# Kernel tuning notes

Measured on AMD Instinct MI355X. Metric: run time of the kernel, lower is better.

Reference implementation:

```python
import jax, jax.numpy as jnp
import numpy as np

C_IN, C_OUT, K = 64, 64, 3
KK = K * K


def _conv3x3(x, w, b):
    # x: [B, Cin, H, W], w: [Cout, Cin, 3, 3], b: [Cout] or None. stride 1, pad 1.
    y = jax.lax.conv_general_dilated(
        x, w, window_strides=(1, 1), padding=((1, 1), (1, 1)),
        dimension_numbers=("NCHW", "OIHW", "NCHW"))
    if b is not None:
        y = y + b[None, :, None, None]
    return y


def _deform_conv2d(x, offset, mask, weight):
    # torchvision.ops.deform_conv2d with stride=1, pad=1, dilation=1, 1 offset group.
    # x: [B,C,H,W]; offset: [B,2*KK,H,W] (per-tap (dy,dx)); mask: [B,KK,H,W];
    # weight: [O,C,K,K]
    B, C, H, W = x.shape
    O = weight.shape[0]
    ky, kx = jnp.meshgrid(jnp.arange(K), jnp.arange(K), indexing="ij")
    hs = jnp.arange(H)
    ws = jnp.arange(W)
    # base sample positions per tap k=(ky*K+kx): [KK,H,W]
    base_y = (hs[:, None] - 1)[None] + ky.reshape(KK, 1, 1)
    base_x = (ws[None, :] - 1)[None] + kx.reshape(KK, 1, 1)
    off = offset.reshape(B, KK, 2, H, W)
    py = base_y[None].astype(x.dtype) + off[:, :, 0]  # [B,KK,H,W]
    px = base_x[None].astype(x.dtype) + off[:, :, 1]

    y0 = jnp.floor(py)
    x0 = jnp.floor(px)
    wy = py - y0  # bilinear fractional weights
    wx = px - x0
    y0i = y0.astype(jnp.int32)
    x0i = x0.astype(jnp.int32)

    imflat = x.reshape(B, C, H * W)

    def gather_b(im, idx):  # im: [C,HW], idx: [KK,H,W] -> [C,KK,H,W]
        return im[:, idx]

    val = jnp.zeros((B, C, KK, H, W), x.dtype)
    for dy, dx in ((0, 0), (0, 1), (1, 0), (1, 1)):
        yc = y0i + dy
        xc = x0i + dx
        valid = ((yc >= 0) & (yc < H) & (xc >= 0) & (xc < W)).astype(x.dtype)
        cw = (wy if dy else (1.0 - wy)) * (wx if dx else (1.0 - wx)) * valid
        idx = jnp.clip(yc, 0, H - 1) * W + jnp.clip(xc, 0, W - 1)
        g = jax.vmap(gather_b)(imflat, idx)  # [B,C,KK,H,W]
        val = val + cw[:, None] * g
    val = val * mask[:, None]  # modulation
    # contract 9-tap patches with conv weight
    return jnp.einsum("bckhw,ock->bohw", val, weight.reshape(O, C, KK))


def setup_inputs() -> dict:
    key = jax.random.key(0)
    ks = jax.random.split(key, 8)
    B, H, W = 4, 96, 96
    cin2 = 2 * C_IN + 2
    frame_i = jax.random.normal(ks[0], (B, C_IN, H, W), jnp.float32)
    frame_j = jax.random.normal(ks[1], (B, C_IN, H, W), jnp.float32)
    flow_ij = jax.random.normal(ks[2], (B, 2, H, W), jnp.float32)
    # small random weights so offsets are nonzero (zero-init would degenerate)
    w_off = jax.random.normal(ks[3], (2 * KK, cin2, K, K), jnp.float32) * 0.01
    b_off = jax.random.normal(ks[4], (2 * KK,), jnp.float32) * 0.1
    w_mod = jax.random.normal(ks[5], (KK, cin2, K, K), jnp.float32) * 0.01
    b_mod = jax.random.normal(ks[6], (KK,), jnp.float32) * 0.1
    w_reg = jax.random.normal(ks[7], (C_OUT, C_IN, K, K), jnp.float32) * (1.0 / np.sqrt(C_IN * KK))
    return {"frame_i": frame_i, "frame_j": frame_j, "flow_ij": flow_ij,
            "w_off": w_off, "b_off": b_off, "w_mod": w_mod, "b_mod": b_mod,
            "w_reg": w_reg}


def reference(frame_i, frame_j, flow_ij, w_off, b_off, w_mod, b_mod, w_reg):
    offset_input = jnp.concatenate([frame_i, frame_j, flow_ij], axis=1)
    offset = _conv3x3(offset_input, w_off, b_off)            # [B,2*KK,H,W]
    modulator = 2.0 * jax.nn.sigmoid(_conv3x3(offset_input, w_mod, b_mod))  # [B,KK,H,W]
    return _deform_conv2d(frame_j, offset, modulator, w_reg)
```

## Files before the change

kernel.cpp:

```cpp
#include <hip/hip_runtime.h>
#include <math.h>

#define BB   4
#define HH   96
#define WW   96
#define HW   (HH * WW)
#define CIN  64
#define COUT 64
#define NPL  17
#define HWP  (HW + 1)
#define NROW (BB * HW)
#define NSTRIP (NROW / 16)
#define BPX3 (NSTRIP / 8)
#define NA   (9 * 5 * 2 * 512)
#define NW   (9 * 2 * 4 * 512)
#define PXB2 (NROW / 32)
#define PWBLK 324
#define TSX  35
#define NIT  (NPL * 54)

typedef short v8s __attribute__((ext_vector_type(8)));
typedef float v4f __attribute__((ext_vector_type(4)));

__device__ __forceinline__ unsigned short f2bf(float f) {
    unsigned u = __float_as_uint(f);
    return (unsigned short)((u + 0x7FFFu + ((u >> 16) & 1u)) >> 16);
}
__device__ __forceinline__ unsigned pack2(float a, float b) {
    return (unsigned)f2bf(a) | ((unsigned)f2bf(b) << 16);
}
__device__ __forceinline__ unsigned bil2(unsigned a, unsigned b, unsigned c,
                                         unsigned d, float w00, float w01,
                                         float w10, float w11) {
    float lo = w00 * __uint_as_float(a << 16) + w01 * __uint_as_float(b << 16)
             + w10 * __uint_as_float(c << 16) + w11 * __uint_as_float(d << 16);
    float hi = w00 * __uint_as_float(a & 0xffff0000u)
             + w01 * __uint_as_float(b & 0xffff0000u)
             + w10 * __uint_as_float(c & 0xffff0000u)
             + w11 * __uint_as_float(d & 0xffff0000u);
    return pack2(lo, hi);
}

__global__ __launch_bounds__(256) void prep_kernel(
    const float* __restrict__ fi, const float* __restrict__ fj,
    const float* __restrict__ fl, const float* __restrict__ w_off,
    const float* __restrict__ w_mod, const float* __restrict__ w_reg,
    uint4* __restrict__ xp, unsigned short* __restrict__ wa2f,
    unsigned short* __restrict__ wb2f)
{
    int blk = blockIdx.x;
    if (blk < PXB2) {
        __shared__ __align__(16) unsigned tile[64 * TSX];
        int tid = threadIdx.x;
        int p = tid & 63, cg = tid >> 6;
        int u = blk >> 1, half = blk & 1;
        int r0 = u * 64;
        int b = r0 / HW;
        int hwb = r0 - b * HW;
        int hw = hwb + p;
        uint4* xpb = xp + (size_t)b * NPL * HWP;
        if (half == 0) {
            const float* pi = fi + (size_t)b * CIN * HW + hw;
#pragma unroll
            for (int d = 0; d < 8; ++d) {
                int c = cg * 16 + 2 * d;
                tile[p * TSX + cg * 8 + d] =
                    pack2(pi[(size_t)c * HW], pi[(size_t)(c + 1) * HW]);
            }
            __syncthreads();
#pragma unroll
            for (int i = 0; i < 2; ++i) {
                int it = i * 256 + tid;
                int pl = it >> 6, rl = it & 63;
                const unsigned* s = &tile[rl * TSX + pl * 4];
                uint4 v = {s[0], s[1], s[2], s[3]};
                xpb[(size_t)pl * HWP + hwb + rl] = v;
            }
        } else {
            const float* pj = fj + (size_t)b * CIN * HW + hw;
#pragma unroll
            for (int d = 0; d < 8; ++d) {
                int c = cg * 16 + 2 * d;
                tile[p * TSX + cg * 8 + d] =
                    pack2(pj[(size_t)c * HW], pj[(size_t)(c + 1) * HW]);
            }
            if (cg == 0) {
                const float* pf = fl + (size_t)b * 2 * HW + hw;
                tile[p * TSX + 32] = pack2(pf[0], pf[HW]);
            }
            __syncthreads();
#pragma unroll
            for (int i = 0; i < 2; ++i) {
                int it = i * 256 + tid;
                int pl = it >> 6, rl = it & 63;
                int o  = (pl >> 1) + (pl & 1) * 4;
                const unsigned* s = &tile[rl * TSX + o * 4];
                uint4 v = {s[0], s[1], s[2], s[3]};
                xpb[(size_t)(8 + pl) * HWP + hwb + rl] = v;
            }
            if (tid < 64) {
                uint4 v = {tile[tid * TSX + 32], 0u, 0u, 0u};
                xpb[(size_t)16 * HWP + hwb + tid] = v;
            }
        }
    } else if (blk < PXB2 + PWBLK) {
        int e = (blk - PXB2) * 256 + threadIdx.x;
        if (e < NA) {
            int t  = e / 5120;
            int r1 = e - t * 5120;
            int ks = r1 >> 10;
            int r2 = r1 & 1023;
            int nt = r2 >> 9;
            int l9 = r2 & 511;
            int l  = l9 >> 3, ee = l9 & 7;
            int m  = l & 15, g = l >> 4;
            int oc = nt * 16 + m;
            int ch = ks * 32 + g * 8 + ee;
            float v = 0.0f;
            if (oc < 27 && ch < 130) {
                if (oc < 18) v = w_off[((size_t)oc * 130 + ch) * 9 + t];
                else         v = w_mod[((size_t)(oc - 18) * 130 + ch) * 9 + t];
            }
            wa2f[e] = f2bf(v);
        } else {
            int e2 = e - NA;
            if (e2 < NW) {
                int k  = e2 >> 12;
                int r1 = e2 & 4095;
                int ks = r1 >> 11;
                int r2 = r1 & 2047;
                int nt = r2 >> 9;
                int l9 = r2 & 511;
                int l  = l9 >> 3, ee = l9 & 7;
                int m  = l & 15, g = l >> 4;
                int o  = nt * 16 + m;
                int c  = ks * 32 + g * 8 + ee;
                wb2f[e2] = f2bf(w_reg[((size_t)o * 64 + c) * 9 + k]);
            }
        }
    } else {
        if (threadIdx.x < BB * NPL) {
            int bz = threadIdx.x / NPL, pl = threadIdx.x - bz * NPL;
            uint4 z = {0u, 0u, 0u, 0u};
            xp[((size_t)bz * NPL + pl) * HWP + HW] = z;
        }
    }
}

__global__ __launch_bounds__(512, 8) void fused_kernel(
    const uint4* __restrict__ xp,
    const unsigned short* __restrict__ wa2f,
    const unsigned short* __restrict__ wb2f,
    const float* __restrict__ b_off, const float* __restrict__ b_mod,
    float* __restrict__ out)
{
    __shared__ __align__(16) unsigned char pool[16384];
    __shared__ __align__(16) float red1[8][8][64];
    __shared__ float lraw[16 * 28];

    uint4* patchL = (uint4*)pool;
    float* red2   = (float*)pool;

    int tid = threadIdx.x;
    int l = tid & 63;
    int wid = __builtin_amdgcn_readfirstlane(tid >> 6);
    int m = l & 15, g = l >> 4;
    int strip = (blockIdx.x & 7) * BPX3 + (blockIdx.x >> 3);
    int b = strip / (HW / 16);
    int hw0 = (strip - b * (HW / 16)) * 16;
    int hw = hw0 + m;
    int x = hw % WW, y = hw / WW;
    int y0b = hw0 / WW, x0b = hw0 - y0b * WW;

    const uint4* xpb = xp + (size_t)b * NPL * HWP;

#pragma unroll
    for (int i = 0; i < 2; ++i) {
        int item = i * 512 + tid;
        if (item < NIT) {
            int pl  = item / 54;
            int rm  = item - pl * 54;
            int run = rm / 18;
            int r18 = rm - run * 18;
            int yy = y0b + run - 1;
            int xx = x0b - 1 + r18;
            bool ok = ((unsigned)yy < HH) && ((unsigned)xx < WW);
            int pos = ok ? (yy * WW + xx) : HW;
            patchL[item] = xpb[(size_t)pl * HWP + pos];
        }
    }
    __syncthreads();

    v4f acc0 = {0.f, 0.f, 0.f, 0.f};
    v4f acc1 = {0.f, 0.f, 0.f, 0.f};
    {
        int nu = (wid < 5) ? 6 : 5;
#pragma unroll
        for (int i = 0; i < 6; ++i) {
            if (i < nu) {
                int u = wid + 8 * i;
                int t = u / 5, ks = u - 5 * t;
                int r = (t / 3) * 18 + (t % 3) + m;
                v8s a;
                if (ks == 4) {
                    uint4 t4 = patchL[16 * 54 + r];
                    if (g) t4 = (uint4){0u, 0u, 0u, 0u};
                    a = __builtin_bit_cast(v8s, t4);
                } else {
                    int pl = (ks == 0) ? g : (ks == 1) ? 4 + g
                           : (ks == 2) ? 8 + 2 * g : 9 + 2 * g;
                    a = *(const v8s*)&patchL[pl * 54 + r];
                }
                const unsigned short* wp =
                    wa2f + ((size_t)(u * 2)) * 512 + l * 8;
                v8s b0 = *(const v8s*)(wp);
                v8s b1 = *(const v8s*)(wp + 512);
                acc0 = __builtin_amdgcn_mfma_f32_16x16x32_bf16(a, b0, acc0, 0, 0, 0);
                acc1 = __builtin_amdgcn_mfma_f32_16x16x32_bf16(a, b1, acc1, 0, 0, 0);
            }
        }
    }

    {
#pragma unroll
        for (int j = 0; j < 4; ++j) red1[wid][j][l] = acc0[j];
#pragma unroll
        for (int j = 0; j < 4; ++j) red1[wid][4 + j][l] = acc1[j];
    }
    __syncthreads();

    {
        int j = wid;
        float v = 0.f;
#pragma unroll
        for (int sw = 0; sw < 8; ++sw) v += red1[sw][j][l];
        int r = j & 3;
        int oc = (j < 4) ? m : 16 + m;
        int pos = g * 4 + r;
        if (oc < 18) {
            lraw[pos * 28 + oc] = v + b_off[oc];
        } else if (oc < 27) {
            lraw[pos * 28 + oc] =
                2.0f / (1.0f + __expf(-(v + b_mod[oc - 18])));
        }
    }
    __syncthreads();

    v4f acc[4];
#pragma unroll
    for (int nt = 0; nt < 4; ++nt) acc[nt] = (v4f){0.f, 0.f, 0.f, 0.f};

    auto do_tap = [&](int k) {
        int ky = k / 3, kx = k - 3 * ky;
        float dy = lraw[m * 28 + 2 * k];
        float dx = lraw[m * 28 + 2 * k + 1];
        float mm = lraw[m * 28 + 18 + k];

        float py = (float)(y - 1 + ky) + dy;
        float px = (float)(x - 1 + kx) + dx;
        float fy = floorf(py), fx = floorf(px);
        int   y0 = (int)fy,    x0 = (int)fx;
        float wy = py - fy,    wx = px - fx;
        int   y1 = y0 + 1,     x1 = x0 + 1;

        bool y0v = (y0 >= 0) && (y0 < HH);
        bool y1v = (y1 >= 0) && (y1 < HH);
        bool x0v = (x0 >= 0) && (x0 < WW);
        bool x1v = (x1 >= 0) && (x1 < WW);

        float w00 = (1.f - wy) * (1.f - wx) * ((y0v && x0v) ? mm : 0.f);
        float w01 = (1.f - wy) * wx         * ((y0v && x1v) ? mm : 0.f);
        float w10 = wy * (1.f - wx)         * ((y1v && x0v) ? mm : 0.f);
        float w11 = wy * wx                 * ((y1v && x1v) ? mm : 0.f);

        int y0c = min(max(y0, 0), HH - 1), y1c = min(max(y1, 0), HH - 1);
        int x0c = min(max(x0, 0), WW - 1), x1c = min(max(x1, 0), WW - 1);
        int i00 = y0c * WW + x0c, i01 = y0c * WW + x1c;
        int i10 = y1c * WW + x0c, i11 = y1c * WW + x1c;

        const uint4* p0 = xpb + (size_t)(8 + 2 * g) * HWP;
        const uint4* p1 = p0 + HWP;

        uint4 a00 = p0[i00];
        uint4 a01 = p0[i01];
        uint4 a10 = p0[i10];
        uint4 a11 = p0[i11];
        uint4 c00 = p1[i00];
        uint4 c01 = p1[i01];
        uint4 c10 = p1[i10];
        uint4 c11 = p1[i11];

        uint4 ov0, ov1;
        ov0.x = bil2(a00.x, a01.x, a10.x, a11.x, w00, w01, w10, w11);
        ov0.y = bil2(a00.y, a01.y, a10.y, a11.y, w00, w01, w10, w11);
        ov0.z = bil2(a00.z, a01.z, a10.z, a11.z, w00, w01, w10, w11);
        ov0.w = bil2(a00.w, a01.w, a10.w, a11.w, w00, w01, w10, w11);
        ov1.x = bil2(c00.x, c01.x, c10.x, c11.x, w00, w01, w10, w11);
        ov1.y = bil2(c00.y, c01.y, c10.y, c11.y, w00, w01, w10, w11);
        ov1.z = bil2(c00.z, c01.z, c10.z, c11.z, w00, w01, w10, w11);
        ov1.w = bil2(c00.w, c01.w, c10.w, c11.w, w00, w01, w10, w11);
        v8s af0 = __builtin_bit_cast(v8s, ov0);
        v8s af1 = __builtin_bit_cast(v8s, ov1);

#pragma unroll
        for (int nt = 0; nt < 4; ++nt) {
            const unsigned short* wp0 =
                wb2f + ((size_t)((k * 2 + 0) * 4 + nt)) * 512 + l * 8;
            const unsigned short* wp1 =
                wb2f + ((size_t)((k * 2 + 1) * 4 + nt)) * 512 + l * 8;
            v8s bb0 = *(const v8s*)wp0;
            v8s bb1 = *(const v8s*)wp1;
            acc[nt] = __builtin_amdgcn_mfma_f32_16x16x32_bf16(af0, bb0, acc[nt], 0, 0, 0);
            acc[nt] = __builtin_amdgcn_mfma_f32_16x16x32_bf16(af1, bb1, acc[nt], 0, 0, 0);
        }
    };

    auto do_half = [&](int k, int ks) {
        int ky = k / 3, kx = k - 3 * ky;
        float dy = lraw[m * 28 + 2 * k];
        float dx = lraw[m * 28 + 2 * k + 1];
        float mm = lraw[m * 28 + 18 + k];

        float py = (float)(y - 1 + ky) + dy;
        float px = (float)(x - 1 + kx) + dx;
        float fy = floorf(py), fx = floorf(px);
        int   y0 = (int)fy,    x0 = (int)fx;
        float wy = py - fy,    wx = px - fx;
        int   y1 = y0 + 1,     x1 = x0 + 1;

        bool y0v = (y0 >= 0) && (y0 < HH);
        bool y1v = (y1 >= 0) && (y1 < HH);
        bool x0v = (x0 >= 0) && (x0 < WW);
        bool x1v = (x1 >= 0) && (x1 < WW);

        float w00 = (1.f - wy) * (1.f - wx) * ((y0v && x0v) ? mm : 0.f);
        float w01 = (1.f - wy) * wx         * ((y0v && x1v) ? mm : 0.f);
        float w10 = wy * (1.f - wx)         * ((y1v && x0v) ? mm : 0.f);
        float w11 = wy * wx                 * ((y1v && x1v) ? mm : 0.f);

        int y0c = min(max(y0, 0), HH - 1), y1c = min(max(y1, 0), HH - 1);
        int x0c = min(max(x0, 0), WW - 1), x1c = min(max(x1, 0), WW - 1);
        int i00 = y0c * WW + x0c, i01 = y0c * WW + x1c;
        int i10 = y1c * WW + x0c, i11 = y1c * WW + x1c;

        const uint4* pk = xpb + (size_t)(8 + 2 * g + ks) * HWP;
        uint4 a00 = pk[i00];
        uint4 a01 = pk[i01];
        uint4 a10 = pk[i10];
        uint4 a11 = pk[i11];

        uint4 ov;
        ov.x = bil2(a00.x, a01.x, a10.x, a11.x, w00, w01, w10, w11);
        ov.y = bil2(a00.y, a01.y, a10.y, a11.y, w00, w01, w10, w11);
        ov.z = bil2(a00.z, a01.z, a10.z, a11.z, w00, w01, w10, w11);
        ov.w = bil2(a00.w, a01.w, a10.w, a11.w, w00, w01, w10, w11);
        v8s af = __builtin_bit_cast(v8s, ov);

#pragma unroll
        for (int nt = 0; nt < 4; ++nt) {
            const unsigned short* wp =
                wb2f + ((size_t)((k * 2 + ks) * 4 + nt)) * 512 + l * 8;
            v8s bb = *(const v8s*)wp;
            acc[nt] = __builtin_amdgcn_mfma_f32_16x16x32_bf16(af, bb, acc[nt], 0, 0, 0);
        }
    };

    do_tap(wid);
    if (wid == 6) do_half(8, 0);
    if (wid == 7) do_half(8, 1);

    if (wid >= 4) {
        float* rb = red2 + ((size_t)(wid - 4) * 16) * 64;
#pragma unroll
        for (int nt = 0; nt < 4; ++nt)
#pragma unroll
            for (int r = 0; r < 4; ++r)
                rb[(nt * 4 + r) * 64 + l] = acc[nt][r];
    }
    __syncthreads();
    if (wid < 4) {
        float* rb = red2 + ((size_t)wid * 16) * 64;
#pragma unroll
        for (int nt = 0; nt < 4; ++nt)
#pragma unroll
            for (int r = 0; r < 4; ++r) {
                float t = rb[(nt * 4 + r) * 64 + l] + acc[nt][r];
                rb[(nt * 4 + r) * 64 + l] = t;
            }
    }
    __syncthreads();
    {
        int nt = wid >> 1, r0 = (wid & 1) * 2;
        float v0 = 0.f, v1 = 0.f;
#pragma unroll
        for (int bu = 0; bu < 4; ++bu) {
            v0 += red2[((size_t)bu * 16 + nt * 4 + r0) * 64 + l];
            v1 += red2[((size_t)bu * 16 + nt * 4 + r0 + 1) * 64 + l];
        }
        float* op = out + ((size_t)(b * COUT + nt * 16 + m)) * HW
                  + hw0 + g * 4 + r0;
        float2 s2 = {v0, v1};
        *(float2*)op = s2;
    }
}

extern "C" void kernel_launch(void* const* d_in, const int* in_sizes, int n_in,
                              void* d_out, int out_size, void* d_ws, size_t ws_size,
                              hipStream_t stream)
{
    const float* frame_i = (const float*)d_in[0];
    const float* frame_j = (const float*)d_in[1];
    const float* flow_ij = (const float*)d_in[2];
    const float* w_off   = (const float*)d_in[3];
    const float* b_off   = (const float*)d_in[4];
    const float* w_mod   = (const float*)d_in[5];
    const float* b_mod   = (const float*)d_in[6];
    const float* w_reg   = (const float*)d_in[7];
    float* out = (float*)d_out;

    uint4* xp = (uint4*)d_ws;
    unsigned short* wa2f = (unsigned short*)(xp + (size_t)BB * NPL * HWP);
    unsigned short* wb2f = wa2f + NA;

    prep_kernel<<<PXB2 + PWBLK + 1, 256, 0, stream>>>(
        frame_i, frame_j, flow_ij, w_off, w_mod, w_reg, xp, wa2f, wb2f);

    fused_kernel<<<NSTRIP, 512, 0, stream>>>(
        xp, wa2f, wb2f, b_off, b_mod, out);
}
```

Before: 112.1 us.

## Merge prep and fused kernels into persistent kernel with grid-wide barrier

Combines the bf16 repacking/weight-prep kernel and the deformable conv kernel into one persistent kernel of 384 blocks. The blocks first do the prep jobs in two halves, then meet at an atomic-counter grid barrier, then loop over the strips. This removes a kernel launch and the gap between launches. In exchange it adds a hipMemsetAsync, a spin barrier that relies on all blocks being resident at once, and lower occupancy from the launch bounds of 512 threads with 4 waves.

```diff
diff --git a/kernel.cpp b/kernel.cpp
--- a/kernel.cpp
+++ b/kernel.cpp
@@ -12,12 +12,14 @@
 #define NROW (BB * HW)
 #define NSTRIP (NROW / 16)
 #define BPX3 (NSTRIP / 8)
+#define GRIDN 384
 #define NA   (9 * 5 * 2 * 512)
 #define NW   (9 * 2 * 4 * 512)
 #define PXB2 (NROW / 32)
 #define PWBLK 324
 #define TSX  35
 #define NIT  (NPL * 54)
+#define CNT_OFF ((size_t)BB * NPL * HWP * 16 + (size_t)NA * 2 + (size_t)NW * 2)
 
 typedef short v8s __attribute__((ext_vector_type(8)));
 typedef float v4f __attribute__((ext_vector_type(4)));
@@ -41,366 +43,383 @@
     return pack2(lo, hi);
 }
 
-__global__ __launch_bounds__(256) void prep_kernel(
+__global__ __launch_bounds__(512, 4) void mono_kernel(
     const float* __restrict__ fi, const float* __restrict__ fj,
     const float* __restrict__ fl, const float* __restrict__ w_off,
     const float* __restrict__ w_mod, const float* __restrict__ w_reg,
+    const float* __restrict__ b_off, const float* __restrict__ b_mod,
     uint4* __restrict__ xp, unsigned short* __restrict__ wa2f,
-    unsigned short* __restrict__ wb2f)
+    unsigned short* __restrict__ wb2f, unsigned* __restrict__ cnt,
+    float* __restrict__ out)
 {
-    int blk = blockIdx.x;
-    if (blk < PXB2) {
-        __shared__ __align__(16) unsigned tile[64 * TSX];
-        int tid = threadIdx.x;
-        int p = tid & 63, cg = tid >> 6;
-        int u = blk >> 1, half = blk & 1;
+    __shared__ __align__(16) unsigned char pool[16384];
+    __shared__ __align__(16) float red1[8][8][64];
+    __shared__ float lraw[16 * 28];
+
+    int tid  = threadIdx.x;
+    int half = tid >> 8;
+    int stid = tid & 255;
+
+#pragma unroll 1
+    for (int it = 0; it < 2; ++it) {
+        int job = it * (GRIDN * 2) + (int)blockIdx.x * 2 + half;
+        unsigned* tile = half ? (unsigned*)red1 : (unsigned*)pool;
+        int p = stid & 63, cgp = stid >> 6;
+        bool isX = job < PXB2;
+        int u = job >> 1;
         int r0 = u * 64;
         int b = r0 / HW;
         int hwb = r0 - b * HW;
         int hw = hwb + p;
         uint4* xpb = xp + (size_t)b * NPL * HWP;
-        if (half == 0) {
+
+        if (isX && half == 0) {
             const float* pi = fi + (size_t)b * CIN * HW + hw;
 #pragma unroll
             for (int d = 0; d < 8; ++d) {
-                int c = cg * 16 + 2 * d;
-                tile[p * TSX + cg * 8 + d] =
+                int c = cgp * 16 + 2 * d;
+                tile[p * TSX + cgp * 8 + d] =
                     pack2(pi[(size_t)c * HW], pi[(size_t)(c + 1) * HW]);
             }
-            __syncthreads();
+        } else if (isX) {
+            const float* pj = fj + (size_t)b * CIN * HW + hw;
+#pragma unroll
+            for (int d = 0; d < 8; ++d) {
+                int c = cgp * 16 + 2 * d;
+                tile[p * TSX + cgp * 8 + d] =
+                    pack2(pj[(size_t)c * HW], pj[(size_t)(c + 1) * HW]);
+            }
+            if (cgp == 0) {
+                const float* pf = fl + (size_t)b * 2 * HW + hw;
+                tile[p * TSX + 32] = pack2(pf[0], pf[HW]);
+            }
+        } else if (job < PXB2 + PWBLK) {
+            int e = (job - PXB2) * 256 + stid;
+            if (e < NA) {
+                int t  = e / 5120;
+                int r1 = e - t * 5120;
+                int ks = r1 >> 10;
+                int r2 = r1 & 1023;
+                int nt = r2 >> 9;
+                int l9 = r2 & 511;
+                int l  = l9 >> 3, ee = l9 & 7;
+                int m  = l & 15, g = l >> 4;
+                int oc = nt * 16 + m;
+                int ch = ks * 32 + g * 8 + ee;
+                float v = 0.0f;
+                if (oc < 27 && ch < 130) {
+                    if (oc < 18) v = w_off[((size_t)oc * 130 + ch) * 9 + t];
+                    else         v = w_mod[((size_t)(oc - 18) * 130 + ch) * 9 + t];
+                }
+                wa2f[e] = f2bf(v);
+            } else {
+                int e2 = e - NA;
+                if (e2 < NW) {
+                    int k  = e2 >> 12;
+                    int r1 = e2 & 4095;
+                    int ks = r1 >> 11;
+                    int r2 = r1 & 2047;
+                    int nt = r2 >> 9;
+                    int l9 = r2 & 511;
+                    int l  = l9 >> 3, ee = l9 & 7;
+                    int m  = l & 15, g = l >> 4;
+                    int o  = nt * 16 + m;
+                    int c  = ks * 32 + g * 8 + ee;
+                    wb2f[e2] = f2bf(w_reg[((size_t)o * 64 + c) * 9 + k]);
+                }
+            }
+        } else if (job == PXB2 + PWBLK) {
+            if (stid < BB * NPL) {
+                int bz = stid / NPL, pl = stid - bz * NPL;
+                uint4 z = {0u, 0u, 0u, 0u};
+                xp[((size_t)bz * NPL + pl) * HWP + HW] = z;
+            }
+        }
+        __syncthreads();
+        if (isX && half == 0) {
 #pragma unroll
             for (int i = 0; i < 2; ++i) {
-                int it = i * 256 + tid;
-                int pl = it >> 6, rl = it & 63;
+                int it2 = i * 256 + stid;
+                int pl = it2 >> 6, rl = it2 & 63;
                 const unsigned* s = &tile[rl * TSX + pl * 4];
                 uint4 v = {s[0], s[1], s[2], s[3]};
                 xpb[(size_t)pl * HWP + hwb + rl] = v;
             }
-        } else {
-            const float* pj = fj + (size_t)b * CIN * HW + hw;
-#pragma unroll
-            for (int d = 0; d < 8; ++d) {
-                int c = cg * 16 + 2 * d;
-                tile[p * TSX + cg * 8 + d] =
-                    pack2(pj[(size_t)c * HW], pj[(size_t)(c + 1) * HW]);
-            }
-            if (cg == 0) {
-                const float* pf = fl + (size_t)b * 2 * HW + hw;
-                tile[p * TSX + 32] = pack2(pf[0], pf[HW]);
-            }
-            __syncthreads();
+        } else if (isX) {
 #pragma unroll
             for (int i = 0; i < 2; ++i) {
-                int it = i * 256 + tid;
-                int pl = it >> 6, rl = it & 63;
+                int it2 = i * 256 + stid;
+                int pl = it2 >> 6, rl = it2 & 63;
                 int o  = (pl >> 1) + (pl & 1) * 4;
                 const unsigned* s = &tile[rl * TSX + o * 4];
                 uint4 v = {s[0], s[1], s[2], s[3]};
                 xpb[(size_t)(8 + pl) * HWP + hwb + rl] = v;
             }
-            if (tid < 64) {
-                uint4 v = {tile[tid * TSX + 32], 0u, 0u, 0u};
-                xpb[(size_t)16 * HWP + hwb + tid] = v;
-            }
-        }
-    } else if (blk < PXB2 + PWBLK) {
-        int e = (blk - PXB2) * 256 + threadIdx.x;
-        if (e < NA) {
-            int t  = e / 5120;
-            int r1 = e - t * 5120;
-            int ks = r1 >> 10;
-            int r2 = r1 & 1023;
-            int nt = r2 >> 9;
-            int l9 = r2 & 511;
-            int l  = l9 >> 3, ee = l9 & 7;
-            int m  = l & 15, g = l >> 4;
-            int oc = nt * 16 + m;
-            int ch = ks * 32 + g * 8 + ee;
-            float v = 0.0f;
-            if (oc < 27 && ch < 130) {
-                if (oc < 18) v = w_off[((size_t)oc * 130 + ch) * 9 + t];
-                else         v = w_mod[((size_t)(oc - 18) * 130 + ch) * 9 + t];
-            }
-            wa2f[e] = f2bf(v);
-        } else {
-            int e2 = e - NA;
-            if (e2 < NW) {
-                int k  = e2 >> 12;
-                int r1 = e2 & 4095;
-                int ks = r1 >> 11;
-                int r2 = r1 & 2047;
-                int nt = r2 >> 9;
-                int l9 = r2 & 511;
-                int l  = l9 >> 3, ee = l9 & 7;
-                int m  = l & 15, g = l >> 4;
-                int o  = nt * 16 + m;
-                int c  = ks * 32 + g * 8 + ee;
-                wb2f[e2] = f2bf(w_reg[((size_t)o * 64 + c) * 9 + k]);
-            }
-        }
-    } else {
-        if (threadIdx.x < BB * NPL) {
-            int bz = threadIdx.x / NPL, pl = threadIdx.x - bz * NPL;
-            uint4 z = {0u, 0u, 0u, 0u};
-            xp[((size_t)bz * NPL + pl) * HWP + HW] = z;
-        }
+            if (stid < 64) {
+                uint4 v = {tile[stid * TSX + 32], 0u, 0u, 0u};
+                xpb[(size_t)16 * HWP + hwb + stid] = v;
+            }
+        }
+        __syncthreads();
     }
-}
-
-__global__ __launch_bounds__(512, 8) void fused_kernel(
-    const uint4* __restrict__ xp,
-    const unsigned short* __restrict__ wa2f,
-    const unsigned short* __restrict__ wb2f,
-    const float* __restrict__ b_off, const float* __restrict__ b_mod,
-    float* __restrict__ out)
-{
-    __shared__ __align__(16) unsigned char pool[16384];
-    __shared__ __align__(16) float red1[8][8][64];
-    __shared__ float lraw[16 * 28];
+
+    if (tid == 0) {
+        __threadfence();
+        __hip_atomic_fetch_add(cnt, 1u, __ATOMIC_ACQ_REL,
+                               __HIP_MEMORY_SCOPE_AGENT);
+        while (__hip_atomic_load(cnt, __ATOMIC_ACQUIRE,
+                                 __HIP_MEMORY_SCOPE_AGENT) < (unsigned)GRIDN)
+            __builtin_amdgcn_s_sleep(2);
+    }
+    __syncthreads();
 
     uint4* patchL = (uint4*)pool;
     float* red2   = (float*)pool;
 
-    int tid = threadIdx.x;
     int l = tid & 63;
     int wid = __builtin_amdgcn_readfirstlane(tid >> 6);
     int m = l & 15, g = l >> 4;
-    int strip = (blockIdx.x & 7) * BPX3 + (blockIdx.x >> 3);
-    int b = strip / (HW / 16);
-    int hw0 = (strip - b * (HW / 16)) * 16;
-    int hw = hw0 + m;
-    int x = hw % WW, y = hw / WW;
-    int y0b = hw0 / WW, x0b = hw0 - y0b * WW;
-
-    const uint4* xpb = xp + (size_t)b * NPL * HWP;
-
-#pragma unroll
-    for (int i = 0; i < 2; ++i) {
-        int item = i * 512 + tid;
-        if (item < NIT) {
-            int pl  = item / 54;
-            int rm  = item - pl * 54;
-            int run = rm / 18;
-            int r18 = rm - run * 18;
-            int yy = y0b + run - 1;
-            int xx = x0b - 1 + r18;
-            bool ok = ((unsigned)yy < HH) && ((unsigned)xx < WW);
-            int pos = ok ? (yy * WW + xx) : HW;
-            patchL[item] = xpb[(size_t)pl * HWP + pos];
-        }
-    }
-    __syncthreads();
-
-    v4f acc0 = {0.f, 0.f, 0.f, 0.f};
-    v4f acc1 = {0.f, 0.f, 0.f, 0.f};
-    {
-        int nu = (wid < 5) ? 6 : 5;
-#pragma unroll
-        for (int i = 0; i < 6; ++i) {
-            if (i < nu) {
-                int u = wid + 8 * i;
-                int t = u / 5, ks = u - 5 * t;
-                int r = (t / 3) * 18 + (t % 3) + m;
-                v8s a;
-                if (ks == 4) {
-                    uint4 t4 = patchL[16 * 54 + r];
-                    if (g) t4 = (uint4){0u, 0u, 0u, 0u};
-                    a = __builtin_bit_cast(v8s, t4);
-                } else {
-                    int pl = (ks == 0) ? g : (ks == 1) ? 4 + g
-                           : (ks == 2) ? 8 + 2 * g : 9 + 2 * g;
-                    a = *(const v8s*)&patchL[pl * 54 + r];
+
+#pragma unroll 1
+    for (int sj = (int)blockIdx.x; sj < NSTRIP; sj += GRIDN) {
+        int strip = (sj & 7) * BPX3 + (sj >> 3);
+        int b = strip / (HW / 16);
+        int hw0 = (strip - b * (HW / 16)) * 16;
+        int hw = hw0 + m;
+        int x = hw % WW, y = hw / WW;
+        int y0b = hw0 / WW, x0b = hw0 - y0b * WW;
+
+        const uint4* xpb = xp + (size_t)b * NPL * HWP;
+
+#pragma unroll
+        for (int i = 0; i < 2; ++i) {
+            int item = i * 512 + tid;
+            if (item < NIT) {
+                int pl  = item / 54;
+                int rm  = item - pl * 54;
+                int run = rm / 18;
+                int r18 = rm - run * 18;
+                int yy = y0b + run - 1;
+                int xx = x0b - 1 + r18;
+                bool ok = ((unsigned)yy < HH) && ((unsigned)xx < WW);
+                int pos = ok ? (yy * WW + xx) : HW;
+                patchL[item] = xpb[(size_t)pl * HWP + pos];
+            }
+        }
+        __syncthreads();
+
+        v4f acc0 = {0.f, 0.f, 0.f, 0.f};
+        v4f acc1 = {0.f, 0.f, 0.f, 0.f};
+        {
+            int nu = (wid < 5) ? 6 : 5;
+#pragma unroll
+            for (int i = 0; i < 6; ++i) {
+                if (i < nu) {
+                    int u = wid + 8 * i;
+                    int t = u / 5, ks = u - 5 * t;
+                    int r = (t / 3) * 18 + (t % 3) + m;
+                    v8s a;
+                    if (ks == 4) {
+                        uint4 t4 = patchL[16 * 54 + r];
+                        if (g) t4 = (uint4){0u, 0u, 0u, 0u};
+                        a = __builtin_bit_cast(v8s, t4);
+                    } else {
+                        int pl = (ks == 0) ? g : (ks == 1) ? 4 + g
+                               : (ks == 2) ? 8 + 2 * g : 9 + 2 * g;
+                        a = *(const v8s*)&patchL[pl * 54 + r];
+                    }
+                    const unsigned short* wp =
+                        wa2f + ((size_t)(u * 2)) * 512 + l * 8;
+                    v8s b0 = *(const v8s*)(wp);
+                    v8s b1 = *(const v8s*)(wp + 512);
+                    acc0 = __builtin_amdgcn_mfma_f32_16x16x32_bf16(a, b0, acc0, 0, 0, 0);
+                    acc1 = __builtin_amdgcn_mfma_f32_16x16x32_bf16(a, b1, acc1, 0, 0, 0);
                 }
+            }
+        }
+
+        {
+#pragma unroll
+            for (int j = 0; j < 4; ++j) red1[wid][j][l] = acc0[j];
+#pragma unroll
+            for (int j = 0; j < 4; ++j) red1[wid][4 + j][l] = acc1[j];
+        }
+        __syncthreads();
+
+        {
+            int j = wid;
+            float v = 0.f;
+#pragma unroll
+            for (int sw = 0; sw < 8; ++sw) v += red1[sw][j][l];
+            int r = j & 3;
+            int oc = (j < 4) ? m : 16 + m;
+            int pos = g * 4 + r;
+            if (oc < 18) {
+                lraw[pos * 28 + oc] = v + b_off[oc];
+            } else if (oc < 27) {
+                lraw[pos * 28 + oc] =
+                    2.0f / (1.0f + __expf(-(v + b_mod[oc - 18])));
+            }
+        }
+        __syncthreads();
+
+        v4f acc[4];
+#pragma unroll
+        for (int nt = 0; nt < 4; ++nt) acc[nt] = (v4f){0.f, 0.f, 0.f, 0.f};
+
+        auto do_tap = [&](int k) {
+            int ky = k / 3, kx = k - 3 * ky;
+            float dy = lraw[m * 28 + 2 * k];
+            float dx = lraw[m * 28 + 2 * k + 1];
+            float mm = lraw[m * 28 + 18 + k];
+
+            float py = (float)(y - 1 + ky) + dy;
+            float px = (float)(x - 1 + kx) + dx;
+            float fy = floorf(py), fx = floorf(px);
+            int   y0 = (int)fy,    x0 = (int)fx;
+            float wy = py - fy,    wx = px - fx;
+            int   y1 = y0 + 1,     x1 = x0 + 1;
+
+            bool y0v = (y0 >= 0) && (y0 < HH);
+            bool y1v = (y1 >= 0) && (y1 < HH);
+            bool x0v = (x0 >= 0) && (x0 < WW);
+            bool x1v = (x1 >= 0) && (x1 < WW);
+
+            float w00 = (1.f - wy) * (1.f - wx) * ((y0v && x0v) ? mm : 0.f);
+            float w01 = (1.f - wy) * wx         * ((y0v && x1v) ? mm : 0.f);
+            float w10 = wy * (1.f - wx)         * ((y1v && x0v) ? mm : 0.f);
+            float w11 = wy * wx                 * ((y1v && x1v) ? mm : 0.f);
+
+            int y0c = min(max(y0, 0), HH - 1), y1c = min(max(y1, 0), HH - 1);
+            int x0c = min(max(x0, 0), WW - 1), x1c = min(max(x1, 0), WW - 1);
+            int i00 = y0c * WW + x0c, i01 = y0c * WW + x1c;
+            int i10 = y1c * WW + x0c, i11 = y1c * WW + x1c;
+
+            const uint4* p0 = xpb + (size_t)(8 + 2 * g) * HWP;
+            const uint4* p1 = p0 + HWP;
+
+            uint4 a00 = p0[i00];
+            uint4 a01 = p0[i01];
+            uint4 a10 = p0[i10];
+            uint4 a11 = p0[i11];
+            uint4 c00 = p1[i00];
+            uint4 c01 = p1[i01];
+            uint4 c10 = p1[i10];
+            uint4 c11 = p1[i11];
+
+            uint4 ov0, ov1;
+            ov0.x = bil2(a00.x, a01.x, a10.x, a11.x, w00, w01, w10, w11);
+            ov0.y = bil2(a00.y, a01.y, a10.y, a11.y, w00, w01, w10, w11);
+            ov0.z = bil2(a00.z, a01.z, a10.z, a11.z, w00, w01, w10, w11);
+            ov0.w = bil2(a00.w, a01.w, a10.w, a11.w, w00, w01, w10, w11);
+            ov1.x = bil2(c00.x, c01.x, c10.x, c11.x, w00, w01, w10, w11);
+            ov1.y = bil2(c00.y, c01.y, c10.y, c11.y, w00, w01, w10, w11);
+            ov1.z = bil2(c00.z, c01.z, c10.z, c11.z, w00, w01, w10, w11);
+            ov1.w = bil2(c00.w, c01.w, c10.w, c11.w, w00, w01, w10, w11);
+            v8s af0 = __builtin_bit_cast(v8s, ov0);
+            v8s af1 = __builtin_bit_cast(v8s, ov1);
+
+#pragma unroll
+            for (int nt = 0; nt < 4; ++nt) {
+                const unsigned short* wp0 =
+                    wb2f + ((size_t)((k * 2 + 0) * 4 + nt)) * 512 + l * 8;
+                const unsigned short* wp1 =
+                    wb2f + ((size_t)((k * 2 + 1) * 4 + nt)) * 512 + l * 8;
+                v8s bb0 = *(const v8s*)wp0;
+                v8s bb1 = *(const v8s*)wp1;
+                acc[nt] = __builtin_amdgcn_mfma_f32_16x16x32_bf16(af0, bb0, acc[nt], 0, 0, 0);
+                acc[nt] = __builtin_amdgcn_mfma_f32_16x16x32_bf16(af1, bb1, acc[nt], 0, 0, 0);
+            }
+        };
+
+        auto do_half = [&](int k, int ks) {
+            int ky = k / 3, kx = k - 3 * ky;
+            float dy = lraw[m * 28 + 2 * k];
+            float dx = lraw[m * 28 + 2 * k + 1];
+            float mm = lraw[m * 28 + 18 + k];
+
+            float py = (float)(y - 1 + ky) + dy;
+            float px = (float)(x - 1 + kx) + dx;
+            float fy = floorf(py), fx = floorf(px);
+            int   y0 = (int)fy,    x0 = (int)fx;
+            float wy = py - fy,    wx = px - fx;
+            int   y1 = y0 + 1,     x1 = x0 + 1;
+
+            bool y0v = (y0 >= 0) && (y0 < HH);
+            bool y1v = (y1 >= 0) && (y1 < HH);
+            bool x0v = (x0 >= 0) && (x0 < WW);
+            bool x1v = (x1 >= 0) && (x1 < WW);
+
+            float w00 = (1.f - wy) * (1.f - wx) * ((y0v && x0v) ? mm : 0.f);
+            float w01 = (1.f - wy) * wx         * ((y0v && x1v) ? mm : 0.f);
+            float w10 = wy * (1.f - wx)         * ((y1v && x0v) ? mm : 0.f);
+            float w11 = wy * wx                 * ((y1v && x1v) ? mm : 0.f);
+
+            int y0c = min(max(y0, 0), HH - 1), y1c = min(max(y1, 0), HH - 1);
+            int x0c = min(max(x0, 0), WW - 1), x1c = min(max(x1, 0), WW - 1);
+            int i00 = y0c * WW + x0c, i01 = y0c * WW + x1c;
+            int i10 = y1c * WW + x0c, i11 = y1c * WW + x1c;
+
+            const uint4* pk = xpb + (size_t)(8 + 2 * g + ks) * HWP;
+            uint4 a00 = pk[i00];
+            uint4 a01 = pk[i01];
+            uint4 a10 = pk[i10];
+            uint4 a11 = pk[i11];
+
+            uint4 ov;
+            ov.x = bil2(a00.x, a01.x, a10.x, a11.x, w00, w01, w10, w11);
+            ov.y = bil2(a00.y, a01.y, a10.y, a11.y, w00, w01, w10, w11);
+            ov.z = bil2(a00.z, a01.z, a10.z, a11.z, w00, w01, w10, w11);
+            ov.w = bil2(a00.w, a01.w, a10.w, a11.w, w00, w01, w10, w11);
+            v8s af = __builtin_bit_cast(v8s, ov);
+
+#pragma unroll
+            for (int nt = 0; nt < 4; ++nt) {
                 const unsigned short* wp =
-                    wa2f + ((size_t)(u * 2)) * 512 + l * 8;
-                v8s b0 = *(const v8s*)(wp);
-                v8s b1 = *(const v8s*)(wp + 512);
-                acc0 = __builtin_amdgcn_mfma_f32_16x16x32_bf16(a, b0, acc0, 0, 0, 0);
-                acc1 = __builtin_amdgcn_mfma_f32_16x16x32_bf16(a, b1, acc1, 0, 0, 0);
-            }
-        }
-    }
-
-    {
-#pragma unroll
-        for (int j = 0; j < 4; ++j) red1[wid][j][l] = acc0[j];
-#pragma unroll
-        for (int j = 0; j < 4; ++j) red1[wid][4 + j][l] = acc1[j];
-    }
-    __syncthreads();
-
-    {
-        int j = wid;
-        float v = 0.f;
-#pragma unroll
-        for (int sw = 0; sw < 8; ++sw) v += red1[sw][j][l];
-        int r = j & 3;
-        int oc = (j < 4) ? m : 16 + m;
-        int pos = g * 4 + r;
-        if (oc < 18) {
-            lraw[pos * 28 + oc] = v + b_off[oc];
-        } else if (oc < 27) {
-            lraw[pos * 28 + oc] =
-                2.0f / (1.0f + __expf(-(v + b_mod[oc - 18])));
-        }
-    }
-    __syncthreads();
-
-    v4f acc[4];
-#pragma unroll
-    for (int nt = 0; nt < 4; ++nt) acc[nt] = (v4f){0.f, 0.f, 0.f, 0.f};
-
-    auto do_tap = [&](int k) {
-        int ky = k / 3, kx = k - 3 * ky;
-        float dy = lraw[m * 28 + 2 * k];
-        float dx = lraw[m * 28 + 2 * k + 1];
-        float mm = lraw[m * 28 + 18 + k];
-
-        float py = (float)(y - 1 + ky) + dy;
-        float px = (float)(x - 1 + kx) + dx;
-        float fy = floorf(py), fx = floorf(px);
-        int   y0 = (int)fy,    x0 = (int)fx;
-        float wy = py - fy,    wx = px - fx;
-        int   y1 = y0 + 1,     x1 = x0 + 1;
-
-        bool y0v = (y0 >= 0) && (y0 < HH);
-        bool y1v = (y1 >= 0) && (y1 < HH);
-        bool x0v = (x0 >= 0) && (x0 < WW);
-        bool x1v = (x1 >= 0) && (x1 < WW);
-
-        float w00 = (1.f - wy) * (1.f - wx) * ((y0v && x0v) ? mm : 0.f);
-        float w01 = (1.f - wy) * wx         * ((y0v && x1v) ? mm : 0.f);
-        float w10 = wy * (1.f - wx)         * ((y1v && x0v) ? mm : 0.f);
-        float w11 = wy * wx                 * ((y1v && x1v) ? mm : 0.f);
-
-        int y0c = min(max(y0, 0), HH - 1), y1c = min(max(y1, 0), HH - 1);
-        int x0c = min(max(x0, 0), WW - 1), x1c = min(max(x1, 0), WW - 1);
-        int i00 = y0c * WW + x0c, i01 = y0c * WW + x1c;
-        int i10 = y1c * WW + x0c, i11 = y1c * WW + x1c;
-
-        const uint4* p0 = xpb + (size_t)(8 + 2 * g) * HWP;
-        const uint4* p1 = p0 + HWP;
-
-        uint4 a00 = p0[i00];
-        uint4 a01 = p0[i01];
-        uint4 a10 = p0[i10];
-        uint4 a11 = p0[i11];
-        uint4 c00 = p1[i00];
-        uint4 c01 = p1[i01];
-        uint4 c10 = p1[i10];
-        uint4 c11 = p1[i11];
-
-        uint4 ov0, ov1;
-        ov0.x = bil2(a00.x, a01.x, a10.x, a11.x, w00, w01, w10, w11);
-        ov0.y = bil2(a00.y, a01.y, a10.y, a11.y, w00, w01, w10, w11);
-        ov0.z = bil2(a00.z, a01.z, a10.z, a11.z, w00, w01, w10, w11);
-        ov0.w = bil2(a00.w, a01.w, a10.w, a11.w, w00, w01, w10, w11);
-        ov1.x = bil2(c00.x, c01.x, c10.x, c11.x, w00, w01, w10, w11);
-        ov1.y = bil2(c00.y, c01.y, c10.y, c11.y, w00, w01, w10, w11);
-        ov1.z = bil2(c00.z, c01.z, c10.z, c11.z, w00, w01, w10, w11);
-        ov1.w = bil2(c00.w, c01.w, c10.w, c11.w, w00, w01, w10, w11);
-        v8s af0 = __builtin_bit_cast(v8s, ov0);
-        v8s af1 = __builtin_bit_cast(v8s, ov1);
-
-#pragma unroll
-        for (int nt = 0; nt < 4; ++nt) {
-            const unsigned short* wp0 =
-                wb2f + ((size_t)((k * 2 + 0) * 4 + nt)) * 512 + l * 8;
-            const unsigned short* wp1 =
-                wb2f + ((size_t)((k * 2 + 1) * 4 + nt)) * 512 + l * 8;
-            v8s bb0 = *(const v8s*)wp0;
-            v8s bb1 = *(const v8s*)wp1;
-            acc[nt] = __builtin_amdgcn_mfma_f32_16x16x32_bf16(af0, bb0, acc[nt], 0, 0, 0);
-            acc[nt] = __builtin_amdgcn_mfma_f32_16x16x32_bf16(af1, bb1, acc[nt], 0, 0, 0);
-        }
-    };
-
-    auto do_half = [&](int k, int ks) {
-        int ky = k / 3, kx = k - 3 * ky;
-        float dy = lraw[m * 28 + 2 * k];
-        float dx = lraw[m * 28 + 2 * k + 1];
-        float mm = lraw[m * 28 + 18 + k];
-
-        float py = (float)(y - 1 + ky) + dy;
-        float px = (float)(x - 1 + kx) + dx;
-        float fy = floorf(py), fx = floorf(px);
-        int   y0 = (int)fy,    x0 = (int)fx;
-        float wy = py - fy,    wx = px - fx;
-        int   y1 = y0 + 1,     x1 = x0 + 1;
-
-        bool y0v = (y0 >= 0) && (y0 < HH);
-        bool y1v = (y1 >= 0) && (y1 < HH);
-        bool x0v = (x0 >= 0) && (x0 < WW);
-        bool x1v = (x1 >= 0) && (x1 < WW);
-
-        float w00 = (1.f - wy) * (1.f - wx) * ((y0v && x0v) ? mm : 0.f);
-        float w01 = (1.f - wy) * wx         * ((y0v && x1v) ? mm : 0.f);
-        float w10 = wy * (1.f - wx)         * ((y1v && x0v) ? mm : 0.f);
-        float w11 = wy * wx                 * ((y1v && x1v) ? mm : 0.f);
-
-        int y0c = min(max(y0, 0), HH - 1), y1c = min(max(y1, 0), HH - 1);
-        int x0c = min(max(x0, 0), WW - 1), x1c = min(max(x1, 0), WW - 1);
-        int i00 = y0c * WW + x0c, i01 = y0c * WW + x1c;
-        int i10 = y1c * WW + x0c, i11 = y1c * WW + x1c;
-
-        const uint4* pk = xpb + (size_t)(8 + 2 * g + ks) * HWP;
-        uint4 a00 = pk[i00];
-        uint4 a01 = pk[i01];
-        uint4 a10 = pk[i10];
-        uint4 a11 = pk[i11];
-
-        uint4 ov;
-        ov.x = bil2(a00.x, a01.x, a10.x, a11.x, w00, w01, w10, w11);
-        ov.y = bil2(a00.y, a01.y, a10.y, a11.y, w00, w01, w10, w11);
-        ov.z = bil2(a00.z, a01.z, a10.z, a11.z, w00, w01, w10, w11);
-        ov.w = bil2(a00.w, a01.w, a10.w, a11.w, w00, w01, w10, w11);
-        v8s af = __builtin_bit_cast(v8s, ov);
-
-#pragma unroll
-        for (int nt = 0; nt < 4; ++nt) {
-            const unsigned short* wp =
-                wb2f + ((size_t)((k * 2 + ks) * 4 + nt)) * 512 + l * 8;
-            v8s bb = *(const v8s*)wp;
-            acc[nt] = __builtin_amdgcn_mfma_f32_16x16x32_bf16(af, bb, acc[nt], 0, 0, 0);
-        }
-    };
-
-    do_tap(wid);
-    if (wid == 6) do_half(8, 0);
-    if (wid == 7) do_half(8, 1);
-
-    if (wid >= 4) {
-        float* rb = red2 + ((size_t)(wid - 4) * 16) * 64;
-#pragma unroll
-        for (int nt = 0; nt < 4; ++nt)
-#pragma unroll
-            for (int r = 0; r < 4; ++r)
-                rb[(nt * 4 + r) * 64 + l] = acc[nt][r];
-    }
-    __syncthreads();
-    if (wid < 4) {
-        float* rb = red2 + ((size_t)wid * 16) * 64;
-#pragma unroll
-        for (int nt = 0; nt < 4; ++nt)
-#pragma unroll
-            for (int r = 0; r < 4; ++r) {
-                float t = rb[(nt * 4 + r) * 64 + l] + acc[nt][r];
-                rb[(nt * 4 + r) * 64 + l] = t;
-            }
-    }
-    __syncthreads();
-    {
-        int nt = wid >> 1, r0 = (wid & 1) * 2;
-        float v0 = 0.f, v1 = 0.f;
-#pragma unroll
-        for (int bu = 0; bu < 4; ++bu) {
-            v0 += red2[((size_t)bu * 16 + nt * 4 + r0) * 64 + l];
-            v1 += red2[((size_t)bu * 16 + nt * 4 + r0 + 1) * 64 + l];
-        }
-        float* op = out + ((size_t)(b * COUT + nt * 16 + m)) * HW
-                  + hw0 + g * 4 + r0;
-        float2 s2 = {v0, v1};
-        *(float2*)op = s2;
+                    wb2f + ((size_t)((k * 2 + ks) * 4 + nt)) * 512 + l * 8;
+                v8s bb = *(const v8s*)wp;
+                acc[nt] = __builtin_amdgcn_mfma_f32_16x16x32_bf16(af, bb, acc[nt], 0, 0, 0);
+            }
+        };
+
+        do_tap(wid);
+        if (wid == 6) do_half(8, 0);
+        if (wid == 7) do_half(8, 1);
+
+        if (wid >= 4) {
+            float* rb = red2 + ((size_t)(wid - 4) * 16) * 64;
+#pragma unroll
+            for (int nt = 0; nt < 4; ++nt)
+#pragma unroll
+                for (int r = 0; r < 4; ++r)
+                    rb[(nt * 4 + r) * 64 + l] = acc[nt][r];
+        }
+        __syncthreads();
+        if (wid < 4) {
+            float* rb = red2 + ((size_t)wid * 16) * 64;
+#pragma unroll
+            for (int nt = 0; nt < 4; ++nt)
+#pragma unroll
+                for (int r = 0; r < 4; ++r) {
+                    float t = rb[(nt * 4 + r) * 64 + l] + acc[nt][r];
+                    rb[(nt * 4 + r) * 64 + l] = t;
+                }
+        }
+        __syncthreads();
+        {
+            int nt = wid >> 1, r0 = (wid & 1) * 2;
+            float v0 = 0.f, v1 = 0.f;
+#pragma unroll
+            for (int bu = 0; bu < 4; ++bu) {
+                v0 += red2[((size_t)bu * 16 + nt * 4 + r0) * 64 + l];
+                v1 += red2[((size_t)bu * 16 + nt * 4 + r0 + 1) * 64 + l];
+            }
+            float* op = out + ((size_t)(b * COUT + nt * 16 + m)) * HW
+                      + hw0 + g * 4 + r0;
+            float2 s2 = {v0, v1};
+            *(float2*)op = s2;
+        }
+        __syncthreads();
     }
 }
 
@@ -421,10 +440,11 @@
     uint4* xp = (uint4*)d_ws;
     unsigned short* wa2f = (unsigned short*)(xp + (size_t)BB * NPL * HWP);
     unsigned short* wb2f = wa2f + NA;
-
-    prep_kernel<<<PXB2 + PWBLK + 1, 256, 0, stream>>>(
-        frame_i, frame_j, flow_ij, w_off, w_mod, w_reg, xp, wa2f, wb2f);
-
-    fused_kernel<<<NSTRIP, 512, 0, stream>>>(
-        xp, wa2f, wb2f, b_off, b_mod, out);
+    unsigned* cnt = (unsigned*)((char*)d_ws + CNT_OFF);
+
+    hipMemsetAsync(cnt, 0, 4, stream);
+
+    mono_kernel<<<GRIDN, 512, 0, stream>>>(
+        frame_i, frame_j, flow_ij, w_off, w_mod, w_reg, b_off, b_mod,
+        xp, wa2f, wb2f, cnt, out);
 }
```

Result: slower. 187.5 us (+67.3%).
